# Kernel tuning notes

Measured on AMD Instinct MI355X. Metric: run time of the kernel, lower is better.

The kernel has to match this reference:

```python
import jax, jax.numpy as jnp
import numpy as np

N = 200000
M0, M1, M2 = 128, 64, 32          # input/output multiplicities for l=0,1,2
H0, H1, H2 = 384, 192, 96         # mlp_mid multiplicities for l=0,1,2
G = H1 + H2                        # number of gate scalars (one per gated channel)
INV_M0 = 1.0 / float(np.sqrt(M0)); INV_M1 = 1.0 / float(np.sqrt(M1)); INV_M2 = 1.0 / float(np.sqrt(M2))
INV_H0 = 1.0 / float(np.sqrt(H0)); INV_H1 = 1.0 / float(np.sqrt(H1)); INV_H2 = 1.0 / float(np.sqrt(H2))


def setup_inputs() -> dict:
    key = jax.random.key(0)
    ks = jax.random.split(key, 12)
    D = M0 + 3 * M1 + 5 * M2  # 480, e3nn layout: [128x0e | 64x1e (64,3) | 32x2e (32,5)]
    node_input = jax.random.normal(ks[0], (N, D), dtype=jnp.float32)
    node_attr = jnp.ones((N, 1), dtype=jnp.float32)  # '1x0e' constant attribute
    # fctp_1 (FCTP + SwishGate): paths l x 0e -> l; extra 0e gate scalars from 0e x 0e
    W0s = jax.random.normal(ks[1], (M0, H0), dtype=jnp.float32)
    b_s = jax.random.normal(ks[2], (H0,), dtype=jnp.float32) * 0.1
    W0g = jax.random.normal(ks[3], (M0, G), dtype=jnp.float32)
    b_g = jax.random.normal(ks[4], (G,), dtype=jnp.float32) * 0.1
    W1 = jax.random.normal(ks[5], (M1, H1), dtype=jnp.float32)
    W2 = jax.random.normal(ks[6], (M2, H2), dtype=jnp.float32)
    # fctp_2 (FCTP, bias on 0e output only)
    V0 = jax.random.normal(ks[7], (H0, M0), dtype=jnp.float32)
    b_o = jax.random.normal(ks[8], (M0,), dtype=jnp.float32) * 0.1
    V1 = jax.random.normal(ks[9], (H1, M1), dtype=jnp.float32)
    V2 = jax.random.normal(ks[10], (H2, M2), dtype=jnp.float32)
    return dict(node_input=node_input, node_attr=node_attr, W0s=W0s, b_s=b_s,
                W0g=W0g, b_g=b_g, W1=W1, W2=W2, V0=V0, b_o=b_o, V1=V1, V2=V2)


def reference(node_input, node_attr, W0s, b_s, W0g, b_g, W1, W2, V0, b_o, V1, V2):
    n = node_input.shape[0]
    x0 = node_input[:, :M0]                                   # [N,128]
    x1 = node_input[:, M0:M0 + 3 * M1].reshape(n, M1, 3)      # [N,64,3]
    x2 = node_input[:, M0 + 3 * M1:].reshape(n, M2, 5)        # [N,32,5]
    y = node_attr                                             # [N,1] scalar attr
    y3 = y[:, :, None]
    # --- fctp_1 + SwishGate (rescale: divide each path by sqrt(fan_in)) ---
    s = jax.nn.silu((x0 @ W0s) * (y * INV_M0) + b_s)          # [N,384] mid scalars
    g = jax.nn.sigmoid((x0 @ W0g) * (y * INV_M0) + b_g)       # [N,288] gates
    v1 = jnp.einsum('num,uw->nwm', x1, W1) * (y3 * INV_M1) * g[:, :H1, None]   # [N,192,3]
    v2 = jnp.einsum('num,uw->nwm', x2, W2) * (y3 * INV_M2) * g[:, H1:, None]   # [N,96,5]
    # --- fctp_2 (bias on scalar output only) ---
    o0 = (s @ V0) * (y * INV_H0) + b_o                        # [N,128]
    o1 = jnp.einsum('num,uw->nwm', v1, V1) * (y3 * INV_H1)    # [N,64,3]
    o2 = jnp.einsum('num,uw->nwm', v2, V2) * (y3 * INV_H2)    # [N,32,5]
    return jnp.concatenate([o0, o1.reshape(n, -1), o2.reshape(n, -1)], axis=-1)  # [N,480]
```

## Files before the change

kernel.cpp:

```cpp
#include <hip/hip_runtime.h>


typedef __attribute__((ext_vector_type(8))) short short8;
typedef __attribute__((ext_vector_type(4))) float f32x4;

#define INV_M0f 0.08838834764831845f
#define INV_M1f 0.125f
#define INV_M2f 0.17677669529663687f
#define INV_H0f 0.05103103630798288f
#define INV_H1f 0.07216878364870323f
#define INV_H2f 0.10206207261596577f

#define OFF_W0T 0
#define OFF_W1T 86016
#define OFF_W2T 98304
#define OFF_V0T 101376
#define OFF_V1T 150528
#define OFF_V2T 162816
#define WP_TOTAL 165888

__device__ __forceinline__ short f2bf_rne(float f) {
    union { float f; unsigned u; } v; v.f = f;
    unsigned r = v.u + 0x7FFFu + ((v.u >> 16) & 1u);
    return (short)(r >> 16);
}
__device__ __forceinline__ short f2bf_fast(float f) {
    unsigned r;
    asm("v_cvt_pk_bf16_f32 %0, %1, %1" : "=v"(r) : "v"(f));
    return (short)r;
}
__device__ __forceinline__ float bf2f(short s) {
    union { unsigned u; float f; } v; v.u = ((unsigned)(unsigned short)s) << 16;
    return v.f;
}

__global__ void prep_weights(const float* __restrict__ W0s, const float* __restrict__ W0g,
                             const float* __restrict__ W1,  const float* __restrict__ W2,
                             const float* __restrict__ V0,  const float* __restrict__ V1,
                             const float* __restrict__ V2,  short* __restrict__ ws)
{
    int i = blockIdx.x * 256 + threadIdx.x;
    if (i < 86016) {
        int j = i >> 7, k = i & 127;
        float v = (j < 384) ? W0s[k * 384 + j] : W0g[k * 288 + (j - 384)];
        ws[i] = f2bf_rne(v * INV_M0f);
    } else if (i < 98304) {
        int e = i - 86016; int w = e >> 6, u = e & 63;
        ws[i] = f2bf_rne(W1[u * 192 + w] * INV_M1f);
    } else if (i < 101376) {
        int e = i - 98304; int w = e >> 5, u = e & 31;
        ws[i] = f2bf_rne(W2[u * 96 + w] * INV_M2f);
    } else if (i < 150528) {
        int e = i - 101376; int j = e / 384, w = e % 384;
        ws[i] = f2bf_rne(V0[w * 128 + j] * INV_H0f);
    } else if (i < 162816) {
        int e = i - 150528; int j = e / 192, w = e % 192;
        ws[i] = f2bf_rne(V1[w * 64 + j] * INV_H1f);
    } else if (i < WP_TOTAL) {
        int e = i - 162816; int j = e / 96, w = e % 96;
        ws[i] = f2bf_rne(V2[w * 32 + j] * INV_H2f);
    }
}

#define X0_STRIDE 136
#define SB_OFF 4352
#define SB_STRIDE 392
#define GT_OFF 16896
#define GT_STRIDE 36
#define UB_OFF 6912
#define UB_STRIDE 200
#define LDS_SHORTS 27264

#define MFMA(a, b, c) __builtin_amdgcn_mfma_f32_16x16x32_bf16((a), (b), (c), 0, 0, 0)

__global__ __launch_bounds__(512, 4) void ffn_main(
    const float* __restrict__ X, const float* __restrict__ Y,
    const float* __restrict__ bs, const float* __restrict__ bg, const float* __restrict__ bo,
    const short* __restrict__ WP, float* __restrict__ out)
{
    __shared__ short lds[LDS_SHORTS];
    short* x0s  = lds;
    short* sbuf = lds + SB_OFF;
    short* gT   = lds + GT_OFF;
    short* x1T  = lds;
    short* x2T  = lds;
    short* ubuf = lds + UB_OFF;

    const int tid  = threadIdx.x;
    const int wid  = tid >> 6;
    const int lane = tid & 63;
    const int m    = lane & 15;
    const int bq   = lane >> 4;
    const int n0   = blockIdx.x * 32;

    short8 w0c[4], w0n[4];
    float bias_c, bias_n;
    {
        const short* w = WP + OFF_W0T + (wid * 16 + m) * 128 + bq * 8;
        #pragma unroll
        for (int k = 0; k < 4; ++k) w0c[k] = *(const short8*)(w + k * 32);
        bias_c = bs[wid * 16 + m];
        const short* w2 = WP + OFF_W0T + ((wid + 8) * 16 + m) * 128 + bq * 8;
        #pragma unroll
        for (int k = 0; k < 4; ++k) w0n[k] = *(const short8*)(w2 + k * 32);
        bias_n = bs[(wid + 8) * 16 + m];
    }

    {
        const int node = tid >> 4, c16 = tid & 15;
        const float* xp = X + (size_t)(n0 + node) * 480 + c16 * 8;
        float4 f0 = *(const float4*)xp;
        float4 f1 = *(const float4*)(xp + 4);
        short8 a;
        a[0]=f2bf_fast(f0.x); a[1]=f2bf_fast(f0.y); a[2]=f2bf_fast(f0.z); a[3]=f2bf_fast(f0.w);
        a[4]=f2bf_fast(f1.x); a[5]=f2bf_fast(f1.y); a[6]=f2bf_fast(f1.z); a[7]=f2bf_fast(f1.w);
        *(short8*)(x0s + node * X0_STRIDE + c16 * 8) = a;
    }

    float yv[2][4];
    #pragma unroll
    for (int t = 0; t < 2; ++t)
        #pragma unroll
        for (int r = 0; r < 4; ++r)
            yv[t][r] = Y[n0 + t * 16 + bq * 4 + r];

    __syncthreads();

    short8 a0[2][4];
    #pragma unroll
    for (int t = 0; t < 2; ++t)
        #pragma unroll
        for (int k = 0; k < 4; ++k)
            a0[t][k] = *(const short8*)(x0s + (t * 16 + m) * X0_STRIDE + k * 32 + bq * 8);

    #pragma unroll 1
    for (int i = 0; i < 6; ++i) {
        const int jt = wid + i * 8;
        if (jt >= 42) break;
        const int jnn = jt + 16;
        short8 w0nn[4];
        float bias_nn = 0.f;
        if (jnn < 42) {
            const short* w = WP + OFF_W0T + (jnn * 16 + m) * 128 + bq * 8;
            #pragma unroll
            for (int k = 0; k < 4; ++k) w0nn[k] = *(const short8*)(w + k * 32);
            bias_nn = (jnn < 24) ? bs[jnn * 16 + m] : bg[(jnn - 24) * 16 + m];
        }
        f32x4 acc0 = {0.f,0.f,0.f,0.f}, acc1 = {0.f,0.f,0.f,0.f};
        #pragma unroll
        for (int k = 0; k < 4; ++k) {
            acc0 = MFMA(a0[0][k], w0c[k], acc0);
            acc1 = MFMA(a0[1][k], w0c[k], acc1);
        }
        if (jt < 24) {
            #pragma unroll
            for (int t = 0; t < 2; ++t) {
                f32x4 acc = t ? acc1 : acc0;
                #pragma unroll
                for (int r = 0; r < 4; ++r) {
                    float val = fmaf(acc[r], yv[t][r], bias_c);
                    float e   = __expf(-val);
                    float sv  = val * __builtin_amdgcn_rcpf(1.f + e);
                    sbuf[(t * 16 + bq * 4 + r) * SB_STRIDE + jt * 16 + m] = f2bf_fast(sv);
                }
            }
        } else {
            const int w = (jt - 24) * 16 + m;
            #pragma unroll
            for (int t = 0; t < 2; ++t) {
                f32x4 acc = t ? acc1 : acc0;
                float sg[4];
                #pragma unroll
                for (int r = 0; r < 4; ++r) {
                    float val = fmaf(acc[r], yv[t][r], bias_c);
                    float e   = __expf(-val);
                    sg[r] = __builtin_amdgcn_rcpf(1.f + e);
                }
                short4 pk;
                pk.x = f2bf_fast(sg[0]); pk.y = f2bf_fast(sg[1]);
                pk.z = f2bf_fast(sg[2]); pk.w = f2bf_fast(sg[3]);
                *(short4*)(gT + w * GT_STRIDE + t * 16 + bq * 4) = pk;
            }
        }
        #pragma unroll
        for (int k = 0; k < 4; ++k) { w0c[k] = w0n[k]; w0n[k] = w0nn[k]; }
        bias_c = bias_n;
        bias_n = bias_nn;
    }

    short8 v0f[12];
    {
        const short* v = WP + OFF_V0T + (wid * 16 + m) * 384 + bq * 8;
        #pragma unroll
        for (int k = 0; k < 12; ++k) v0f[k] = *(const short8*)(v + k * 32);
    }
    const float bo_r = bo[wid * 16 + m];
    __syncthreads();

    {
        f32x4 accD0 = {0.f,0.f,0.f,0.f}, accD1 = {0.f,0.f,0.f,0.f};
        #pragma unroll
        for (int k = 0; k < 12; ++k) {
            short8 sa0 = *(const short8*)(sbuf + m * SB_STRIDE + k * 32 + bq * 8);
            short8 sa1 = *(const short8*)(sbuf + (16 + m) * SB_STRIDE + k * 32 + bq * 8);
            accD0 = MFMA(sa0, v0f[k], accD0);
            accD1 = MFMA(sa1, v0f[k], accD1);
        }
        #pragma unroll
        for (int t = 0; t < 2; ++t) {
            f32x4 acc = t ? accD1 : accD0;
            #pragma unroll
            for (int r = 0; r < 4; ++r)
                out[(size_t)(n0 + t * 16 + bq * 4 + r) * 480 + wid * 16 + m] =
                    fmaf(acc[r], yv[t][r], bo_r);
        }
    }

    short8 w1f[2][2];
    #pragma unroll
    for (int jj = 0; jj < 2; ++jj) {
        const int jt = wid + jj * 8;
        if (jt < 12) {
            const short* w = WP + OFF_W1T + (jt * 16 + m) * 64 + bq * 8;
            w1f[jj][0] = *(const short8*)(w);
            w1f[jj][1] = *(const short8*)(w + 32);
        }
    }
    short8 v1f[6];
    if (wid >= 4) {
        const short* v = WP + OFF_V1T + ((wid - 4) * 16 + m) * 192 + bq * 8;
        #pragma unroll
        for (int k = 0; k < 6; ++k) v1f[k] = *(const short8*)(v + k * 32);
    }
    __syncthreads();

    {
        const int node = tid >> 4, c16 = tid & 15;
        const float* xp = X + (size_t)(n0 + node) * 480 + 128 + c16 * 12;
        float4 fa = *(const float4*)xp;
        float4 fb = *(const float4*)(xp + 4);
        float4 fc = *(const float4*)(xp + 8);
        float vals[12] = {fa.x,fa.y,fa.z,fa.w, fb.x,fb.y,fb.z,fb.w, fc.x,fc.y,fc.z,fc.w};
        #pragma unroll
        for (int mmv = 0; mmv < 3; ++mmv) {
            short4 s4;
            s4.x = f2bf_fast(vals[mmv]);
            s4.y = f2bf_fast(vals[mmv + 3]);
            s4.z = f2bf_fast(vals[mmv + 6]);
            s4.w = f2bf_fast(vals[mmv + 9]);
            *(short4*)(x1T + mmv * 2304 + node * 72 + c16 * 4) = s4;
        }
    }
    __syncthreads();

    float o1a[3][2][4];
    #pragma unroll
    for (int mm = 0; mm < 3; ++mm) {
        #pragma unroll
        for (int jj = 0; jj < 2; ++jj) {
            const int jt = wid + jj * 8;
            if (jt < 12) {
                f32x4 accA = {0.f,0.f,0.f,0.f}, accB = {0.f,0.f,0.f,0.f};
                short8 a00 = *(const short8*)(x1T + mm * 2304 + m * 72 + bq * 8);
                short8 a01 = *(const short8*)(x1T + mm * 2304 + m * 72 + 32 + bq * 8);
                short8 a10 = *(const short8*)(x1T + mm * 2304 + (16 + m) * 72 + bq * 8);
                short8 a11 = *(const short8*)(x1T + mm * 2304 + (16 + m) * 72 + 32 + bq * 8);
                accA = MFMA(a00, w1f[jj][0], accA);
                accA = MFMA(a01, w1f[jj][1], accA);
                accB = MFMA(a10, w1f[jj][0], accB);
                accB = MFMA(a11, w1f[jj][1], accB);
                const int w = jt * 16 + m;
                #pragma unroll
                for (int t = 0; t < 2; ++t) {
                    f32x4 acc = t ? accB : accA;
                    short4 g4 = *(const short4*)(gT + w * GT_STRIDE + t * 16 + bq * 4);
                    #pragma unroll
                    for (int r = 0; r < 4; ++r) {
                        const int node = t * 16 + bq * 4 + r;
                        float gv = bf2f(r == 0 ? g4.x : r == 1 ? g4.y : r == 2 ? g4.z : g4.w);
                        ubuf[node * UB_STRIDE + w] =
                            f2bf_fast(acc[r] * yv[t][r] * gv);
                    }
                }
            }
        }
        __syncthreads();
        if (wid >= 4) {
            f32x4 accA = {0.f,0.f,0.f,0.f}, accB = {0.f,0.f,0.f,0.f};
            #pragma unroll
            for (int k = 0; k < 6; ++k) {
                short8 au0 = *(const short8*)(ubuf + m * UB_STRIDE + k * 32 + bq * 8);
                short8 au1 = *(const short8*)(ubuf + (16 + m) * UB_STRIDE + k * 32 + bq * 8);
                accA = MFMA(au0, v1f[k], accA);
                accB = MFMA(au1, v1f[k], accB);
            }
            #pragma unroll
            for (int t = 0; t < 2; ++t) {
                f32x4 acc = t ? accB : accA;
                #pragma unroll
                for (int r = 0; r < 4; ++r)
                    o1a[mm][t][r] = acc[r] * yv[t][r];
            }
        }
        __syncthreads();
    }
    if (wid >= 4) {
        const int jc = (wid - 4) * 16 + m;
        #pragma unroll
        for (int t = 0; t < 2; ++t)
            #pragma unroll
            for (int r = 0; r < 4; ++r) {
                float* p = out + (size_t)(n0 + t * 16 + bq * 4 + r) * 480 + 128 + jc * 3;
                p[0] = o1a[0][t][r]; p[1] = o1a[1][t][r]; p[2] = o1a[2][t][r];
            }
    }

    short8 w2f;
    if (wid < 6)
        w2f = *(const short8*)(WP + OFF_W2T + (wid * 16 + m) * 32 + bq * 8);
    short8 v2f[3];
    if (wid >= 6) {
        const short* v = WP + OFF_V2T + ((wid - 6) * 16 + m) * 96 + bq * 8;
        #pragma unroll
        for (int k = 0; k < 3; ++k) v2f[k] = *(const short8*)(v + k * 32);
    }

    {
        const int node = tid >> 4, c16 = tid & 15;
        const float* xp = X + (size_t)(n0 + node) * 480 + 320 + c16 * 10;
        float vals[10];
        #pragma unroll
        for (int p = 0; p < 5; ++p) {
            float2 f = *(const float2*)(xp + p * 2);
            vals[p * 2] = f.x; vals[p * 2 + 1] = f.y;
        }
        #pragma unroll
        for (int mmv = 0; mmv < 5; ++mmv) {
            short2 s2;
            s2.x = f2bf_fast(vals[mmv]);
            s2.y = f2bf_fast(vals[mmv + 5]);
            *(short2*)(x2T + mmv * 1280 + node * 40 + c16 * 2) = s2;
        }
    }
    __syncthreads();

    float o2a[5][2][4];
    #pragma unroll
    for (int mm = 0; mm < 5; ++mm) {
        if (wid < 6) {
            f32x4 accA = {0.f,0.f,0.f,0.f}, accB = {0.f,0.f,0.f,0.f};
            short8 a20 = *(const short8*)(x2T + mm * 1280 + m * 40 + bq * 8);
            short8 a21 = *(const short8*)(x2T + mm * 1280 + (16 + m) * 40 + bq * 8);
            accA = MFMA(a20, w2f, accA);
            accB = MFMA(a21, w2f, accB);
            const int w = 192 + wid * 16 + m;
            #pragma unroll
            for (int t = 0; t < 2; ++t) {
                f32x4 acc = t ? accB : accA;
                short4 g4 = *(const short4*)(gT + w * GT_STRIDE + t * 16 + bq * 4);
                #pragma unroll
                for (int r = 0; r < 4; ++r) {
                    const int node = t * 16 + bq * 4 + r;
                    float gv = bf2f(r == 0 ? g4.x : r == 1 ? g4.y : r == 2 ? g4.z : g4.w);
                    ubuf[node * UB_STRIDE + wid * 16 + m] =
                        f2bf_fast(acc[r] * yv[t][r] * gv);
                }
            }
        }
        __syncthreads();
        if (wid >= 6) {
            f32x4 accA = {0.f,0.f,0.f,0.f}, accB = {0.f,0.f,0.f,0.f};
            #pragma unroll
            for (int k = 0; k < 3; ++k) {
                short8 au0 = *(const short8*)(ubuf + m * UB_STRIDE + k * 32 + bq * 8);
                short8 au1 = *(const short8*)(ubuf + (16 + m) * UB_STRIDE + k * 32 + bq * 8);
                accA = MFMA(au0, v2f[k], accA);
                accB = MFMA(au1, v2f[k], accB);
            }
            #pragma unroll
            for (int t = 0; t < 2; ++t) {
                f32x4 acc = t ? accB : accA;
                #pragma unroll
                for (int r = 0; r < 4; ++r)
                    o2a[mm][t][r] = acc[r] * yv[t][r];
            }
        }
        if (mm < 4) __syncthreads();
    }
    if (wid >= 6) {
        const int jc = (wid - 6) * 16 + m;
        #pragma unroll
        for (int t = 0; t < 2; ++t)
            #pragma unroll
            for (int r = 0; r < 4; ++r) {
                float* p = out + (size_t)(n0 + t * 16 + bq * 4 + r) * 480 + 320 + jc * 5;
                p[0] = o2a[0][t][r]; p[1] = o2a[1][t][r]; p[2] = o2a[2][t][r];
                p[3] = o2a[3][t][r]; p[4] = o2a[4][t][r];
            }
    }
}

extern "C" void kernel_launch(void* const* d_in, const int* in_sizes, int n_in,
                              void* d_out, int out_size, void* d_ws, size_t ws_size,
                              hipStream_t stream)
{
    const float* X   = (const float*)d_in[0];
    const float* Y   = (const float*)d_in[1];
    const float* W0s = (const float*)d_in[2];
    const float* bs  = (const float*)d_in[3];
    const float* W0g = (const float*)d_in[4];
    const float* bg  = (const float*)d_in[5];
    const float* W1  = (const float*)d_in[6];
    const float* W2  = (const float*)d_in[7];
    const float* V0  = (const float*)d_in[8];
    const float* bo  = (const float*)d_in[9];
    const float* V1  = (const float*)d_in[10];
    const float* V2  = (const float*)d_in[11];
    short* WP  = (short*)d_ws;
    float* out = (float*)d_out;

    const int n = in_sizes[0] / 480;
    const int tiles = n / 32;

    prep_weights<<<dim3((WP_TOTAL + 255) / 256), dim3(256), 0, stream>>>(
        W0s, W0g, W1, W2, V0, V1, V2, WP);
    ffn_main<<<dim3(tiles), dim3(512), 0, stream>>>(X, Y, bs, bg, bo, WP, out);
}
```

Before: 322.9 us.

## Buffer per-component intermediates to cut barriers and overlap l=2 loads with l=1 output

Gives each spatial component of the l=1 and l=2 intermediates its own LDS plane, so all three (or five) components are written before a single barrier and read afterward. This removes the per-component barrier pairs. Warps 0-3 now load and convert the l=2 input while warps 4-7 finish and store the l=1 output, and the W2/V2 fragment loads move earlier. The cost is a larger LDS footprint (about 73KB per block versus 54KB), which may reduce how many blocks fit on a CU.

```diff
diff --git a/kernel.cpp b/kernel.cpp
--- a/kernel.cpp
+++ b/kernel.cpp
@@ -65,11 +65,15 @@
 #define X0_STRIDE 136
 #define SB_OFF 4352
 #define SB_STRIDE 392
-#define GT_OFF 16896
+#define GT_OFF 26112
 #define GT_STRIDE 36
-#define UB_OFF 6912
-#define UB_STRIDE 200
-#define LDS_SHORTS 27264
+#define UB1_OFF 6912
+#define UB1_PLANE 6400
+#define UB1_STRIDE 200
+#define UB2_OFF 6400
+#define UB2_PLANE 3328
+#define UB2_STRIDE 104
+#define LDS_SHORTS 36480
 
 #define MFMA(a, b, c) __builtin_amdgcn_mfma_f32_16x16x32_bf16((a), (b), (c), 0, 0, 0)
 
@@ -79,12 +83,13 @@
     const short* __restrict__ WP, float* __restrict__ out)
 {
     __shared__ short lds[LDS_SHORTS];
-    short* x0s  = lds;
-    short* sbuf = lds + SB_OFF;
-    short* gT   = lds + GT_OFF;
-    short* x1T  = lds;
-    short* x2T  = lds;
-    short* ubuf = lds + UB_OFF;
+    short* x0s   = lds;
+    short* sbuf  = lds + SB_OFF;
+    short* gT    = lds + GT_OFF;
+    short* x1T   = lds;
+    short* x2T   = lds;
+    short* ubuf1 = lds + UB1_OFF;
+    short* ubuf2 = lds + UB2_OFF;
 
     const int tid  = threadIdx.x;
     const int wid  = tid >> 6;
@@ -232,6 +237,15 @@
         #pragma unroll
         for (int k = 0; k < 6; ++k) v1f[k] = *(const short8*)(v + k * 32);
     }
+    short8 w2f;
+    if (wid < 6)
+        w2f = *(const short8*)(WP + OFF_W2T + (wid * 16 + m) * 32 + bq * 8);
+    short8 v2f[3];
+    if (wid >= 6) {
+        const short* v = WP + OFF_V2T + ((wid - 6) * 16 + m) * 96 + bq * 8;
+        #pragma unroll
+        for (int k = 0; k < 3; ++k) v2f[k] = *(const short8*)(v + k * 32);
+    }
     __syncthreads();
 
     {
@@ -253,7 +267,6 @@
     }
     __syncthreads();
 
-    float o1a[3][2][4];
     #pragma unroll
     for (int mm = 0; mm < 3; ++mm) {
         #pragma unroll
@@ -278,19 +291,24 @@
                     for (int r = 0; r < 4; ++r) {
                         const int node = t * 16 + bq * 4 + r;
                         float gv = bf2f(r == 0 ? g4.x : r == 1 ? g4.y : r == 2 ? g4.z : g4.w);
-                        ubuf[node * UB_STRIDE + w] =
+                        ubuf1[mm * UB1_PLANE + node * UB1_STRIDE + w] =
                             f2bf_fast(acc[r] * yv[t][r] * gv);
                     }
                 }
             }
         }
-        __syncthreads();
-        if (wid >= 4) {
+    }
+    __syncthreads();
+
+    if (wid >= 4) {
+        float o1a[3][2][4];
+        #pragma unroll
+        for (int mm = 0; mm < 3; ++mm) {
             f32x4 accA = {0.f,0.f,0.f,0.f}, accB = {0.f,0.f,0.f,0.f};
             #pragma unroll
             for (int k = 0; k < 6; ++k) {
-                short8 au0 = *(const short8*)(ubuf + m * UB_STRIDE + k * 32 + bq * 8);
-                short8 au1 = *(const short8*)(ubuf + (16 + m) * UB_STRIDE + k * 32 + bq * 8);
+                short8 au0 = *(const short8*)(ubuf1 + mm * UB1_PLANE + m * UB1_STRIDE + k * 32 + bq * 8);
+                short8 au1 = *(const short8*)(ubuf1 + mm * UB1_PLANE + (16 + m) * UB1_STRIDE + k * 32 + bq * 8);
                 accA = MFMA(au0, v1f[k], accA);
                 accB = MFMA(au1, v1f[k], accB);
             }
@@ -302,9 +320,6 @@
                     o1a[mm][t][r] = acc[r] * yv[t][r];
             }
         }
-        __syncthreads();
-    }
-    if (wid >= 4) {
         const int jc = (wid - 4) * 16 + m;
         #pragma unroll
         for (int t = 0; t < 2; ++t)
@@ -313,46 +328,37 @@
                 float* p = out + (size_t)(n0 + t * 16 + bq * 4 + r) * 480 + 128 + jc * 3;
                 p[0] = o1a[0][t][r]; p[1] = o1a[1][t][r]; p[2] = o1a[2][t][r];
             }
-    }
-
-    short8 w2f;
-    if (wid < 6)
-        w2f = *(const short8*)(WP + OFF_W2T + (wid * 16 + m) * 32 + bq * 8);
-    short8 v2f[3];
-    if (wid >= 6) {
-        const short* v = WP + OFF_V2T + ((wid - 6) * 16 + m) * 96 + bq * 8;
-        #pragma unroll
-        for (int k = 0; k < 3; ++k) v2f[k] = *(const short8*)(v + k * 32);
-    }
-
-    {
-        const int node = tid >> 4, c16 = tid & 15;
-        const float* xp = X + (size_t)(n0 + node) * 480 + 320 + c16 * 10;
-        float vals[10];
+    } else {
+        const int node2 = tid >> 3;
+        const int c8 = tid & 7;
+        const float* xp2 = X + (size_t)(n0 + node2) * 480 + 320 + c8 * 20;
+        float vals[20];
         #pragma unroll
         for (int p = 0; p < 5; ++p) {
-            float2 f = *(const float2*)(xp + p * 2);
-            vals[p * 2] = f.x; vals[p * 2 + 1] = f.y;
+            float4 f = *(const float4*)(xp2 + p * 4);
+            vals[p * 4] = f.x; vals[p * 4 + 1] = f.y;
+            vals[p * 4 + 2] = f.z; vals[p * 4 + 3] = f.w;
         }
         #pragma unroll
         for (int mmv = 0; mmv < 5; ++mmv) {
-            short2 s2;
-            s2.x = f2bf_fast(vals[mmv]);
-            s2.y = f2bf_fast(vals[mmv + 5]);
-            *(short2*)(x2T + mmv * 1280 + node * 40 + c16 * 2) = s2;
-        }
-    }
-    __syncthreads();
-
-    float o2a[5][2][4];
-    #pragma unroll
-    for (int mm = 0; mm < 5; ++mm) {
-        if (wid < 6) {
-            f32x4 accA = {0.f,0.f,0.f,0.f}, accB = {0.f,0.f,0.f,0.f};
+            short4 s4;
+            s4.x = f2bf_fast(vals[mmv]);
+            s4.y = f2bf_fast(vals[mmv + 5]);
+            s4.z = f2bf_fast(vals[mmv + 10]);
+            s4.w = f2bf_fast(vals[mmv + 15]);
+            *(short4*)(x2T + mmv * 1280 + node2 * 40 + c8 * 4) = s4;
+        }
+    }
+    __syncthreads();
+
+    if (wid < 6) {
+        #pragma unroll
+        for (int mm = 0; mm < 5; ++mm) {
+            f32x4 zz = {0.f,0.f,0.f,0.f};
             short8 a20 = *(const short8*)(x2T + mm * 1280 + m * 40 + bq * 8);
             short8 a21 = *(const short8*)(x2T + mm * 1280 + (16 + m) * 40 + bq * 8);
-            accA = MFMA(a20, w2f, accA);
-            accB = MFMA(a21, w2f, accB);
+            f32x4 accA = MFMA(a20, w2f, zz);
+            f32x4 accB = MFMA(a21, w2f, zz);
             const int w = 192 + wid * 16 + m;
             #pragma unroll
             for (int t = 0; t < 2; ++t) {
@@ -362,18 +368,23 @@
                 for (int r = 0; r < 4; ++r) {
                     const int node = t * 16 + bq * 4 + r;
                     float gv = bf2f(r == 0 ? g4.x : r == 1 ? g4.y : r == 2 ? g4.z : g4.w);
-                    ubuf[node * UB_STRIDE + wid * 16 + m] =
+                    ubuf2[mm * UB2_PLANE + node * UB2_STRIDE + wid * 16 + m] =
                         f2bf_fast(acc[r] * yv[t][r] * gv);
                 }
             }
         }
-        __syncthreads();
-        if (wid >= 6) {
+    }
+    __syncthreads();
+
+    if (wid >= 6) {
+        float o2a[5][2][4];
+        #pragma unroll
+        for (int mm = 0; mm < 5; ++mm) {
             f32x4 accA = {0.f,0.f,0.f,0.f}, accB = {0.f,0.f,0.f,0.f};
             #pragma unroll
             for (int k = 0; k < 3; ++k) {
-                short8 au0 = *(const short8*)(ubuf + m * UB_STRIDE + k * 32 + bq * 8);
-                short8 au1 = *(const short8*)(ubuf + (16 + m) * UB_STRIDE + k * 32 + bq * 8);
+                short8 au0 = *(const short8*)(ubuf2 + mm * UB2_PLANE + m * UB2_STRIDE + k * 32 + bq * 8);
+                short8 au1 = *(const short8*)(ubuf2 + mm * UB2_PLANE + (16 + m) * UB2_STRIDE + k * 32 + bq * 8);
                 accA = MFMA(au0, v2f[k], accA);
                 accB = MFMA(au1, v2f[k], accB);
             }
@@ -385,9 +396,6 @@
                     o2a[mm][t][r] = acc[r] * yv[t][r];
             }
         }
-        if (mm < 4) __syncthreads();
-    }
-    if (wid >= 6) {
         const int jc = (wid - 6) * 16 + m;
         #pragma unroll
         for (int t = 0; t < 2; ++t)
```

Measured after the change: 314.2 us (median of 2 runs). -2.7%, faster.
